# Optimization experiments

Hardware: AMD Instinct MI355X
Metric: run time of the kernel (lower is better)

The kernel has to match this reference:

```python
import jax, jax.numpy as jnp
import numpy as np

EPS_DIST = 1e-10
BN_EPS = 1e-5
K = 3  # nsample / three_nn


def setup_inputs() -> dict:
    key = jax.random.key(0)
    ks = jax.random.split(key, 8)
    B, N, S, D1, D2 = 4, 8192, 2048, 128, 256
    C_in = D1 + D2  # 384
    H = 256
    inp = {
        "pos1": jax.random.normal(ks[0], (B, 3, N), dtype=jnp.float32),
        "pos2": jax.random.normal(ks[1], (B, 3, S), dtype=jnp.float32),
        "feature1": jax.random.normal(ks[2], (B, D1, N), dtype=jnp.float32),
        "feature2": jax.random.normal(ks[3], (B, D2, S), dtype=jnp.float32),
        # MLP layer 1: Conv1d(384->256, k=1) + BN
        "W1": jax.random.normal(ks[4], (H, C_in), dtype=jnp.float32) * (1.0 / np.sqrt(C_in)),
        "b1": jnp.zeros((H,), dtype=jnp.float32),
        "g1": jnp.ones((H,), dtype=jnp.float32),
        "be1": jnp.zeros((H,), dtype=jnp.float32),
        # MLP layer 2: Conv1d(256->256, k=1) + BN
        "W2": jax.random.normal(ks[5], (H, H), dtype=jnp.float32) * (1.0 / np.sqrt(H)),
        "b2": jnp.zeros((H,), dtype=jnp.float32),
        "g2": jnp.ones((H,), dtype=jnp.float32),
        "be2": jnp.zeros((H,), dtype=jnp.float32),
    }
    return inp


def _conv_bn_relu(x, W, b, gamma, beta):
    # x: [B, Cin, N]; 1x1 Conv1d == channel GEMM
    y = jnp.einsum("oc,bcn->bon", W, x) + b[None, :, None]
    # BatchNorm1d in training mode: batch statistics over (B, N)
    mean = jnp.mean(y, axis=(0, 2), keepdims=True)
    var = jnp.mean(jnp.square(y - mean), axis=(0, 2), keepdims=True)
    y = (y - mean) * jax.lax.rsqrt(var + BN_EPS)
    y = y * gamma[None, :, None] + beta[None, :, None]
    return jax.nn.relu(y)


def reference(pos1, pos2, feature1, feature2, W1, b1, g1, be1, W2, b2, g2, be2):
    # pos1: [B,3,N], pos2: [B,3,S], feature1: [B,D1,N], feature2: [B,D2,S]
    p1 = jnp.swapaxes(pos1, 1, 2)  # [B,N,3]
    p2 = jnp.swapaxes(pos2, 1, 2)  # [B,S,3]
    # three_nn: squared-distance 3-NN of each point in p1 among p2
    d2 = (jnp.sum(p1 * p1, -1)[:, :, None]
          + jnp.sum(p2 * p2, -1)[:, None, :]
          - 2.0 * jnp.einsum("bnc,bsc->bns", p1, p2))  # [B,N,S]
    neg_vals, idx = jax.lax.top_k(-d2, K)  # idx: [B,N,3]
    dists = jnp.maximum(-neg_vals, EPS_DIST)  # dists[dists<1e-10]=1e-10
    w = 1.0 / dists
    w = w / jnp.sum(w, -1, keepdims=True)  # [B,N,3]
    # grouping_operation: gather feature2 [B,D,S] by idx -> [B,D,N,3]
    grouped = jax.vmap(lambda f, i: f[:, i])(feature2, idx)
    interpolated = jnp.sum(grouped * w[:, None, :, :], axis=-1)  # [B,D2,N]
    feat = jnp.concatenate([interpolated, feature1], axis=1)  # [B,384,N]
    feat = _conv_bn_relu(feat, W1, b1, g1, be1)
    feat = _conv_bn_relu(feat, W2, b2, g2, be2)
    return feat  # [B,256,N]
```

## Files before the change

kernel.cpp:

```cpp
#include <hip/hip_runtime.h>
#include <hip/hip_bf16.h>
#include <cstdint>

typedef unsigned short u16;
typedef unsigned int u32;
typedef unsigned long long u64;
typedef __bf16 bf16x8 __attribute__((ext_vector_type(8)));
typedef float f32x4 __attribute__((ext_vector_type(4)));
typedef u16 u16x8 __attribute__((ext_vector_type(8)));

__device__ __forceinline__ u16 f2b(float f) {
    unsigned int u = __float_as_uint(f);
    u += 0x7fffu + ((u >> 16) & 1u);
    return (u16)(u >> 16);
}
__device__ __forceinline__ float b2f(u16 h) {
    return __uint_as_float(((unsigned int)h) << 16);
}
__device__ __forceinline__ void async_cp16(void* lds, const void* g) {
    __builtin_amdgcn_global_load_lds((const __attribute__((address_space(1))) void*)g,
                                     (__attribute__((address_space(3))) void*)lds, 16, 0, 0);
}
__device__ __forceinline__ u32 fmono(float f) {
    u32 u = __float_as_uint(f);
    return u ^ (((u32)((int)u >> 31)) | 0x80000000u);
}
__device__ __forceinline__ u64 shfl_xor_u64(u64 v, int mask) {
    u32 lo = (u32)v, hi = (u32)(v >> 32);
    lo = (u32)__shfl_xor((int)lo, mask);
    hi = (u32)__shfl_xor((int)hi, mask);
    return ((u64)hi << 32) | lo;
}
__device__ __forceinline__ void ins3(u64 k, u64& k0, u64& k1, u64& k2) {
    bool c0 = k > k0, c1 = k > k1, c2 = k > k2;
    k2 = c1 ? k1 : (c2 ? k : k2);
    k1 = c0 ? k0 : (c1 ? k : k1);
    k0 = c0 ? k : k0;
}
__device__ __forceinline__ int pkix(int i) { return i + (i >> 6); }

#define NB_NN  512
#define NB_CVT 160
#define NB_T2  512
#define NB_T1  1024

__global__ __launch_bounds__(256, 4) void prep_kernel(const float* __restrict__ w1,
                                                      const float* __restrict__ w2,
                                                      u16* __restrict__ wb,
                                                      const float* __restrict__ feature2,
                                                      u16* __restrict__ f2t,
                                                      const float* __restrict__ feature1,
                                                      u16* __restrict__ f1t,
                                                      const float* __restrict__ pos1,
                                                      const float* __restrict__ pos2,
                                                      int* __restrict__ idx_out,
                                                      float* __restrict__ w_out) {
    __shared__ __align__(16) char smem[22784];
    int bi = blockIdx.x;
    int tid = threadIdx.x;

    if (bi >= NB_NN) {
        int ci = bi - NB_NN;
        if (ci < NB_CVT) {
            int i = ci * 256 + tid;
            if (i < 40960) {
                const float* src = (i < 24576) ? w1 : w2;
                int k = (i < 24576) ? i : (i - 24576);
                float4 v = *(const float4*)&src[(size_t)k * 4];
                ushort4 o;
                o.x = f2b(v.x); o.y = f2b(v.y); o.z = f2b(v.z); o.w = f2b(v.w);
                *(ushort4*)&wb[(size_t)i * 4] = o;
            }
            return;
        }
        float (*t)[65] = (float (*)[65])smem;
        const float* in; u16* out; int C, S, s0, c0, b;
        if (ci < NB_CVT + NB_T2) {
            int lin = ci - NB_CVT;
            C = 256; S = 2048; in = feature2; out = f2t;
            s0 = (lin & 31) * 64; c0 = ((lin >> 5) & 3) * 64; b = lin >> 7;
        } else {
            int lin = ci - NB_CVT - NB_T2;
            C = 128; S = 8192; in = feature1; out = f1t;
            s0 = (lin & 127) * 64; c0 = ((lin >> 7) & 1) * 64; b = lin >> 8;
        }
        const float* ib = in + (size_t)b * C * S;
        u16* ob = out + (size_t)b * S * C;
        int col = tid & 63, r0 = tid >> 6;
#pragma unroll
        for (int p = 0; p < 16; ++p) {
            int c = p * 4 + r0;
            t[c][col] = ib[(size_t)(c0 + c) * S + s0 + col];
        }
        __syncthreads();
#pragma unroll
        for (int p = 0; p < 16; ++p) {
            int s = p * 4 + r0;
            ob[(size_t)(s0 + s) * C + c0 + col] = f2b(t[col][s]);
        }
        return;
    }

    float4* pk = (float4*)smem;
    u64* warr = (u64*)(smem + 16640);
    int j0 = bi * 64;
    int b = j0 >> 13;
    const float* p2 = pos2 + (size_t)b * 3 * 2048;
    int p = tid & 15, ck = tid >> 4;
    int wv = tid >> 6, lane = tid & 63;
    const float* p1 = pos1 + (size_t)b * 3 * 8192;
    float qx[4], qy[4], qz[4];
#pragma unroll
    for (int t = 0; t < 4; ++t) {
        int n = (j0 & 8191) + p + t * 16;
        qx[t] = p1[n]; qy[t] = p1[8192 + n]; qz[t] = p1[16384 + n];
    }
    u64 key[4][3];
#pragma unroll
    for (int t = 0; t < 4; ++t) { key[t][0] = 0; key[t][1] = 0; key[t][2] = 0; }

    for (int half = 0; half < 2; ++half) {
        int hbase = half * 1024;
        for (int i = tid; i < 1024; i += 256) {
            int s = hbase + i;
            float x = p2[s], y = p2[2048 + s], z = p2[4096 + s];
            pk[pkix(i)] = make_float4(x, y, z, -0.5f * (x * x + y * y + z * z));
        }
        __syncthreads();

        float g[4][3]; int id[4][3];
#pragma unroll
        for (int t = 0; t < 4; ++t) {
            g[t][0] = -3.4e38f; g[t][1] = -3.4e38f; g[t][2] = -3.4e38f;
            id[t][0] = 0; id[t][1] = 0; id[t][2] = 0;
        }
        int sb = ck * 64;
        const float4* pc = pk + pkix(sb);
#pragma unroll 2
        for (int it = 0; it < 64; ++it) {
            float4 cd = pc[it];
            int s = sb + it;
#pragma unroll
            for (int t = 0; t < 4; ++t) {
                float tv = fmaf(qx[t], cd.x, fmaf(qy[t], cd.y, fmaf(qz[t], cd.z, cd.w)));
                bool c0 = tv > g[t][0], c1 = tv > g[t][1], c2 = tv > g[t][2];
                g[t][2] = c1 ? g[t][1] : (c2 ? tv : g[t][2]);
                id[t][2] = c1 ? id[t][1] : (c2 ? s : id[t][2]);
                g[t][1] = c0 ? g[t][0] : (c1 ? tv : g[t][1]);
                id[t][1] = c0 ? id[t][0] : (c1 ? s : id[t][1]);
                g[t][0] = c0 ? tv : g[t][0];
                id[t][0] = c0 ? s : id[t][0];
            }
        }
        __syncthreads();

#pragma unroll
        for (int t = 0; t < 4; ++t) {
#pragma unroll
            for (int r = 0; r < 3; ++r)
                ins3(((u64)fmono(g[t][r]) << 32) | (u64)(2047 - (hbase + id[t][r])),
                     key[t][0], key[t][1], key[t][2]);
        }
    }

#pragma unroll
    for (int mask = 16; mask <= 32; mask <<= 1) {
#pragma unroll
        for (int t = 0; t < 4; ++t) {
            u64 m0 = shfl_xor_u64(key[t][0], mask);
            u64 m1 = shfl_xor_u64(key[t][1], mask);
            u64 m2 = shfl_xor_u64(key[t][2], mask);
            ins3(m0, key[t][0], key[t][1], key[t][2]);
            ins3(m1, key[t][0], key[t][1], key[t][2]);
            ins3(m2, key[t][0], key[t][1], key[t][2]);
        }
    }
    if (lane < 16) {
        u64* wr = &warr[(wv * 16 + p) * 12];
#pragma unroll
        for (int t = 0; t < 4; ++t) {
            wr[t * 3 + 0] = key[t][0]; wr[t * 3 + 1] = key[t][1]; wr[t * 3 + 2] = key[t][2];
        }
    }
    __syncthreads();
    if (tid < 64) {
        int pp = tid & 15, t = tid >> 4;
        const u64* w0 = &warr[pp * 12 + t * 3];
        u64 k0 = w0[0], k1 = w0[1], k2 = w0[2];
#pragma unroll
        for (int w = 1; w < 4; ++w) {
            const u64* wr = &warr[(w * 16 + pp) * 12 + t * 3];
            ins3(wr[0], k0, k1, k2);
            ins3(wr[1], k0, k1, k2);
            ins3(wr[2], k0, k1, k2);
        }
        int s0 = 2047 - (int)(k0 & 0xFFFFFFFFu);
        int s1 = 2047 - (int)(k1 & 0xFFFFFFFFu);
        int s2 = 2047 - (int)(k2 & 0xFFFFFFFFu);
        int j = j0 + pp + t * 16;
        int n = j & 8191;
        float x1 = p1[n], y1 = p1[8192 + n], z1 = p1[16384 + n];
        float n1 = x1 * x1 + y1 * y1 + z1 * z1;
        float X0 = p2[s0], Y0 = p2[2048 + s0], Z0 = p2[4096 + s0];
        float X1 = p2[s1], Y1v = p2[2048 + s1], Z1 = p2[4096 + s1];
        float X2 = p2[s2], Y2v = p2[2048 + s2], Z2 = p2[4096 + s2];
        float t0 = x1 * X0 + y1 * Y0 + z1 * Z0 - 0.5f * (X0 * X0 + Y0 * Y0 + Z0 * Z0);
        float t1 = x1 * X1 + y1 * Y1v + z1 * Z1 - 0.5f * (X1 * X1 + Y1v * Y1v + Z1 * Z1);
        float t2 = x1 * X2 + y1 * Y2v + z1 * Z2 - 0.5f * (X2 * X2 + Y2v * Y2v + Z2 * Z2);
        float d0 = fmaxf(fmaf(-2.f, t0, n1), 1e-10f);
        float d1 = fmaxf(fmaf(-2.f, t1, n1), 1e-10f);
        float d2 = fmaxf(fmaf(-2.f, t2, n1), 1e-10f);
        float w0v = 1.f / d0, w1v = 1.f / d1, w2v = 1.f / d2;
        float inv = 1.f / (w0v + w1v + w2v);
        idx_out[j * 3] = s0; idx_out[j * 3 + 1] = s1; idx_out[j * 3 + 2] = s2;
        w_out[j * 3] = w0v * inv; w_out[j * 3 + 1] = w1v * inv; w_out[j * 3 + 2] = w2v * inv;
    }
}

template <int KT, bool GATHER, bool FUSE>
__global__ __launch_bounds__(256, 2) void gemm_kernel(const u16* __restrict__ A1,
                                                      const u16* __restrict__ A2,
                                                      const u16* __restrict__ Bw,
                                                      const float* __restrict__ bias,
                                                      const int* __restrict__ idx,
                                                      const float* __restrict__ wgt,
                                                      const float* __restrict__ stats_in,
                                                      const float* __restrict__ g_in,
                                                      const float* __restrict__ be_in,
                                                      u16* __restrict__ Yb,
                                                      float* __restrict__ stats) {
    __shared__ __align__(16) char smemA[36864];
    u16* Al = (u16*)smemA;
    u16* Bl = (u16*)(smemA + 16384);
    u16* T  = (u16*)smemA;
    float2* BNT = (float2*)(smemA + 34816);
    int tid = threadIdx.x;
    int lane = tid & 63, wv = tid >> 6;
    int j0 = blockIdx.x * 128, m0 = blockIdx.y * 128;
    int l15 = lane & 15, q = lane >> 4;
    int wj = (wv >> 1) * 64, wm = (wv & 1) * 64;
    f32x4 acc[4][4];
#pragma unroll
    for (int i = 0; i < 4; ++i)
#pragma unroll
        for (int jj = 0; jj < 4; ++jj) acc[i][jj] = (f32x4){0.f, 0.f, 0.f, 0.f};

    int rbase = wv * 32;
    int lrow = lane >> 3, lchunk = lane & 7;
    const u16* Bg = Bw + (size_t)m0 * KT;

    if (FUSE) {
        int m = tid;
        const float inv = 1.f / 32768.f;
        float mean = stats_in[m] * inv;
        float var = stats_in[256 + m] * inv - mean * mean;
        float a = g_in[m] * rsqrtf(var + 1e-5f);
        BNT[m] = make_float2(a, be_in[m] - mean * a);
        __syncthreads();
    }

    const u16* grow0[4]; const u16* grow1[4]; const u16* grow2[4];
    float gw0[4], gw1[4], gw2[4];
    if (GATHER) {
#pragma unroll
        for (int qq = 0; qq < 4; ++qq) {
            int jl = rbase + qq * 8 + lrow;
            int j = j0 + jl;
            int bb = j >> 13;
            const u16* fb = A1 + (size_t)bb * 2048 * 256;
            grow0[qq] = fb + (size_t)idx[j * 3 + 0] * 256;
            grow1[qq] = fb + (size_t)idx[j * 3 + 1] * 256;
            grow2[qq] = fb + (size_t)idx[j * 3 + 2] * 256;
            gw0[qq] = wgt[j * 3 + 0]; gw1[qq] = wgt[j * 3 + 1]; gw2[qq] = wgt[j * 3 + 2];
        }
    }

    for (int k0 = 0; k0 < KT; k0 += 64) {
        if (GATHER && k0 < 256) {
            int c = k0 + lchunk * 8;
#pragma unroll
            for (int qq = 0; qq < 4; ++qq) {
                int row = rbase + qq * 8;
                u16x8 v0 = *(const u16x8*)(grow0[qq] + c);
                u16x8 v1 = *(const u16x8*)(grow1[qq] + c);
                u16x8 v2 = *(const u16x8*)(grow2[qq] + c);
                u16x8 o;
#pragma unroll
                for (int e = 0; e < 8; ++e)
                    o[e] = f2b(gw0[qq] * b2f(v0[e]) + gw1[qq] * b2f(v1[e]) + gw2[qq] * b2f(v2[e]));
                *(u16x8*)&Al[(row + lrow) * 64 + lchunk * 8] = o;
                async_cp16(&Bl[row * 64], Bg + (size_t)(row + lrow) * KT + k0 + lchunk * 8);
            }
        } else if (FUSE) {
            int c = k0 + lchunk * 8;
            float2 bn[8];
#pragma unroll
            for (int e = 0; e < 8; ++e) bn[e] = BNT[c + e];
#pragma unroll
            for (int qq = 0; qq < 4; ++qq) {
                int row = rbase + qq * 8;
                u16x8 y = *(const u16x8*)&A1[(size_t)(j0 + row + lrow) * 256 + c];
                u16x8 o;
#pragma unroll
                for (int e = 0; e < 8; ++e)
                    o[e] = f2b(fmaxf(b2f(y[e]) * bn[e].x + bn[e].y, 0.f));
                *(u16x8*)&Al[(row + lrow) * 64 + lchunk * 8] = o;
                async_cp16(&Bl[row * 64], Bg + (size_t)(row + lrow) * KT + k0 + lchunk * 8);
            }
        } else {
            const u16* src = A2 + (size_t)j0 * 128 + (k0 - 256);
#pragma unroll
            for (int qq = 0; qq < 4; ++qq) {
                int row = rbase + qq * 8;
                async_cp16(&Al[row * 64], src + (size_t)(row + lrow) * 128 + lchunk * 8);
                async_cp16(&Bl[row * 64], Bg + (size_t)(row + lrow) * KT + k0 + lchunk * 8);
            }
        }
        __syncthreads();
#pragma unroll
        for (int ks = 0; ks < 2; ++ks) {
            bf16x8 af[4], bfr[4];
#pragma unroll
            for (int i = 0; i < 4; ++i)
                af[i] = *(const bf16x8*)&Al[(wj + i * 16 + l15) * 64 + ks * 32 + q * 8];
#pragma unroll
            for (int i = 0; i < 4; ++i)
                bfr[i] = *(const bf16x8*)&Bl[(wm + i * 16 + l15) * 64 + ks * 32 + q * 8];
#pragma unroll
            for (int i = 0; i < 4; ++i)
#pragma unroll
                for (int jj = 0; jj < 4; ++jj)
                    acc[i][jj] = __builtin_amdgcn_mfma_f32_16x16x32_bf16(af[i], bfr[jj],
                                                                         acc[i][jj], 0, 0, 0);
        }
        __syncthreads();
    }
#pragma unroll
    for (int jj = 0; jj < 4; ++jj) {
        int ml = wm + jj * 16 + l15;
        float bv = bias[m0 + ml];
        float s = 0.f, s2 = 0.f;
#pragma unroll
        for (int i = 0; i < 4; ++i) {
            int jl = wj + i * 16 + q * 4;
#pragma unroll
            for (int r = 0; r < 4; ++r) {
                float v = acc[i][jj][r] + bv;
                s += v; s2 += v * v;
                T[(jl + r) * 136 + ml] = f2b(v);
            }
        }
        s += __shfl_xor(s, 16); s += __shfl_xor(s, 32);
        s2 += __shfl_xor(s2, 16); s2 += __shfl_xor(s2, 32);
        if (q == 0) {
            atomicAdd(&stats[m0 + ml], s);
            atomicAdd(&stats[256 + m0 + ml], s2);
        }
    }
    __syncthreads();
#pragma unroll
    for (int it = 0; it < 8; ++it) {
        int jl = it * 16 + wv * 4 + q;
        u16x8 v = *(const u16x8*)&T[jl * 136 + l15 * 8];
        *(u16x8*)&Yb[(size_t)(j0 + jl) * 256 + m0 + l15 * 8] = v;
    }
}

__global__ __launch_bounds__(256) void final_out_kernel(const u16* __restrict__ Y2,
                                                        const float* __restrict__ stats,
                                                        const float* __restrict__ g,
                                                        const float* __restrict__ be,
                                                        float* __restrict__ out) {
    __shared__ float t[64][65];
    int j0 = blockIdx.x * 64, o0 = blockIdx.y * 64;
    int tid = threadIdx.x;
    int c4 = (tid & 15) * 4, rw = tid >> 4;
#pragma unroll
    for (int p = 0; p < 4; ++p) {
        int jl = p * 16 + rw;
        ushort4 v = *(const ushort4*)&Y2[(size_t)(j0 + jl) * 256 + o0 + c4];
        t[jl][c4] = b2f(v.x); t[jl][c4 + 1] = b2f(v.y);
        t[jl][c4 + 2] = b2f(v.z); t[jl][c4 + 3] = b2f(v.w);
    }
    __syncthreads();
    int b = j0 >> 13, n0 = j0 & 8191;
    const float inv = 1.f / 32768.f;
#pragma unroll
    for (int p = 0; p < 4; ++p) {
        int ol = p * 16 + rw;
        int o = o0 + ol;
        float mean = stats[o] * inv;
        float var = stats[256 + o] * inv - mean * mean;
        float a = g[o] * rsqrtf(var + 1e-5f);
        float s = be[o] - mean * a;
        float4 v;
        v.x = fmaxf(t[c4][ol] * a + s, 0.f);
        v.y = fmaxf(t[c4 + 1][ol] * a + s, 0.f);
        v.z = fmaxf(t[c4 + 2][ol] * a + s, 0.f);
        v.w = fmaxf(t[c4 + 3][ol] * a + s, 0.f);
        *(float4*)&out[(size_t)b * 2097152 + (size_t)o * 8192 + n0 + c4] = v;
    }
}

extern "C" void kernel_launch(void* const* d_in, const int* in_sizes, int n_in,
                              void* d_out, int out_size, void* d_ws, size_t ws_size,
                              hipStream_t stream) {
    const float* pos1 = (const float*)d_in[0];
    const float* pos2 = (const float*)d_in[1];
    const float* feature1 = (const float*)d_in[2];
    const float* feature2 = (const float*)d_in[3];
    const float* W1 = (const float*)d_in[4];
    const float* b1 = (const float*)d_in[5];
    const float* g1 = (const float*)d_in[6];
    const float* be1 = (const float*)d_in[7];
    const float* W2 = (const float*)d_in[8];
    const float* b2 = (const float*)d_in[9];
    const float* g2 = (const float*)d_in[10];
    const float* be2 = (const float*)d_in[11];

    char* ws = (char*)d_ws;
    int*   IDX    = (int*)(ws + 0);
    float* WGT    = (float*)(ws + 393216);
    u16*   W1B    = (u16*)(ws + 786432);
    u16*   W2B    = (u16*)(ws + 983040);
    float* STATS  = (float*)(ws + 1114112);
    u16*   F2T    = (u16*)(ws + 1118208);
    u16*   F1T    = (u16*)(ws + 5312512);
    u16*   Y1     = (u16*)(ws + 13701120);
    u16*   Y2     = (u16*)(ws + 30478336);
    float* OUT    = (float*)d_out;

    hipMemsetAsync(STATS, 0, 1024 * sizeof(float), stream);
    prep_kernel<<<NB_NN + NB_CVT + NB_T2 + NB_T1, 256, 0, stream>>>(
        W1, W2, W1B, feature2, F2T, feature1, F1T, pos1, pos2, IDX, WGT);
    gemm_kernel<384, true, false><<<dim3(256, 2), 256, 0, stream>>>(
        F2T, F1T, W1B, b1, IDX, WGT, nullptr, nullptr, nullptr, Y1, STATS);
    gemm_kernel<256, false, true><<<dim3(256, 2), 256, 0, stream>>>(
        Y1, nullptr, W2B, b2, nullptr, nullptr, STATS, g1, be1, Y2, STATS + 512);
    final_out_kernel<<<dim3(512, 4), 256, 0, stream>>>(Y2, STATS + 512, g2, be2, OUT);
}
```

Before: 199.3 us.

## Double-buffer A tile in LDS and load weight fragments directly to registers

The GEMM main loop now double-buffers the A (activation) tile in LDS. The next K-slice is staged (gather/BN-fuse/async copy) while MFMAs run on the current buffer, so only one barrier per iteration remains. Weight (B) fragments are loaded straight from global memory into registers instead of through LDS, which frees LDS space for the second A buffer. This trades more global loads per wave (the weights are re-read by each wave, with uncoalesced row access) and higher register pressure for overlap of the A staging with compute.

```diff
diff --git a/kernel.cpp b/kernel.cpp
--- a/kernel.cpp
+++ b/kernel.cpp
@@ -229,11 +229,10 @@
                                                       const float* __restrict__ be_in,
                                                       u16* __restrict__ Yb,
                                                       float* __restrict__ stats) {
-    __shared__ __align__(16) char smemA[36864];
+    __shared__ __align__(16) char smemA[34816];
     u16* Al = (u16*)smemA;
-    u16* Bl = (u16*)(smemA + 16384);
     u16* T  = (u16*)smemA;
-    float2* BNT = (float2*)(smemA + 34816);
+    float2* BNT = (float2*)(smemA + 32768);
     int tid = threadIdx.x;
     int lane = tid & 63, wv = tid >> 6;
     int j0 = blockIdx.x * 128, m0 = blockIdx.y * 128;
@@ -275,9 +274,10 @@
         }
     }
 
-    for (int k0 = 0; k0 < KT; k0 += 64) {
-        if (GATHER && k0 < 256) {
-            int c = k0 + lchunk * 8;
+    auto stageA = [&](int k0s, int bsel) {
+        u16* dst = Al + bsel * 8192;
+        if (GATHER && k0s < 256) {
+            int c = k0s + lchunk * 8;
 #pragma unroll
             for (int qq = 0; qq < 4; ++qq) {
                 int row = rbase + qq * 8;
@@ -288,11 +288,10 @@
 #pragma unroll
                 for (int e = 0; e < 8; ++e)
                     o[e] = f2b(gw0[qq] * b2f(v0[e]) + gw1[qq] * b2f(v1[e]) + gw2[qq] * b2f(v2[e]));
-                *(u16x8*)&Al[(row + lrow) * 64 + lchunk * 8] = o;
-                async_cp16(&Bl[row * 64], Bg + (size_t)(row + lrow) * KT + k0 + lchunk * 8);
+                *(u16x8*)&dst[(row + lrow) * 64 + lchunk * 8] = o;
             }
         } else if (FUSE) {
-            int c = k0 + lchunk * 8;
+            int c = k0s + lchunk * 8;
             float2 bn[8];
 #pragma unroll
             for (int e = 0; e < 8; ++e) bn[e] = BNT[c + e];
@@ -304,34 +303,45 @@
 #pragma unroll
                 for (int e = 0; e < 8; ++e)
                     o[e] = f2b(fmaxf(b2f(y[e]) * bn[e].x + bn[e].y, 0.f));
-                *(u16x8*)&Al[(row + lrow) * 64 + lchunk * 8] = o;
-                async_cp16(&Bl[row * 64], Bg + (size_t)(row + lrow) * KT + k0 + lchunk * 8);
+                *(u16x8*)&dst[(row + lrow) * 64 + lchunk * 8] = o;
             }
         } else {
-            const u16* src = A2 + (size_t)j0 * 128 + (k0 - 256);
+            const u16* src = A2 + (size_t)j0 * 128 + (k0s - 256);
 #pragma unroll
             for (int qq = 0; qq < 4; ++qq) {
                 int row = rbase + qq * 8;
-                async_cp16(&Al[row * 64], src + (size_t)(row + lrow) * 128 + lchunk * 8);
-                async_cp16(&Bl[row * 64], Bg + (size_t)(row + lrow) * KT + k0 + lchunk * 8);
-            }
-        }
-        __syncthreads();
+                async_cp16(&dst[row * 64], src + (size_t)(row + lrow) * 128 + lchunk * 8);
+            }
+        }
+    };
+
+    constexpr int NI = KT / 64;
+    stageA(0, 0);
+    __syncthreads();
+#pragma unroll
+    for (int i = 0; i < NI; ++i) {
+        int k0 = i * 64;
+        bf16x8 breg[2][4];
+#pragma unroll
+        for (int ks = 0; ks < 2; ++ks)
+#pragma unroll
+            for (int jj = 0; jj < 4; ++jj)
+                breg[ks][jj] = *(const bf16x8*)&Bg[(size_t)(wm + jj * 16 + l15) * KT +
+                                                   k0 + ks * 32 + q * 8];
+        if (i + 1 < NI) stageA(k0 + 64, (i + 1) & 1);
+        const u16* buf = Al + (i & 1) * 8192;
 #pragma unroll
         for (int ks = 0; ks < 2; ++ks) {
-            bf16x8 af[4], bfr[4];
-#pragma unroll
-            for (int i = 0; i < 4; ++i)
-                af[i] = *(const bf16x8*)&Al[(wj + i * 16 + l15) * 64 + ks * 32 + q * 8];
-#pragma unroll
-            for (int i = 0; i < 4; ++i)
-                bfr[i] = *(const bf16x8*)&Bl[(wm + i * 16 + l15) * 64 + ks * 32 + q * 8];
-#pragma unroll
-            for (int i = 0; i < 4; ++i)
+            bf16x8 af[4];
+#pragma unroll
+            for (int ii = 0; ii < 4; ++ii)
+                af[ii] = *(const bf16x8*)&buf[(wj + ii * 16 + l15) * 64 + ks * 32 + q * 8];
+#pragma unroll
+            for (int ii = 0; ii < 4; ++ii)
 #pragma unroll
                 for (int jj = 0; jj < 4; ++jj)
-                    acc[i][jj] = __builtin_amdgcn_mfma_f32_16x16x32_bf16(af[i], bfr[jj],
-                                                                         acc[i][jj], 0, 0, 0);
+                    acc[ii][jj] = __builtin_amdgcn_mfma_f32_16x16x32_bf16(af[ii], breg[ks][jj],
+                                                                          acc[ii][jj], 0, 0, 0);
         }
         __syncthreads();
     }
```

After: 207.7 us. 4.2% more time.
